# Kernel optimization log

Hardware: AMD Instinct MI355X
Metric: run time of the kernel (lower is better)

Reference implementation:

```python
import jax, jax.numpy as jnp
import numpy as np

B, N, F_IN = 32, 512, 64
HEADS = (8, 8)
HIDS = (64, 64)
EDGE_P = 0.05  # graph density
NEG_SLOPE = 0.2
NEG_INF = -1e20


def setup_inputs() -> dict:
    key = jax.random.key(0)
    ks = jax.random.split(key, 8)
    x = jax.random.normal(ks[0], (B, N, F_IN), dtype=jnp.float32)
    adj = (jax.random.uniform(ks[1], (B, N, N)) < EDGE_P).astype(jnp.float32)
    adj = jnp.maximum(adj, adj.transpose(0, 2, 1))  # symmetric adjacency
    # mask = (batch, row): every (b, n) pair gets the masked softmax
    b_idx = jnp.repeat(jnp.arange(B, dtype=jnp.int32), N)   # [B*N]
    r_idx = jnp.tile(jnp.arange(N, dtype=jnp.int32), B)     # [B*N]
    # layer 0: f_in=64 -> f_out=64, H=8 ; layer 1: f_in=64*8=512 -> f_out=64, H=8
    W0 = jax.random.normal(ks[2], (F_IN, HIDS[0]), dtype=jnp.float32) / jnp.sqrt(jnp.float32(F_IN))
    a_src0 = jax.random.normal(ks[3], (HIDS[0], HEADS[0]), dtype=jnp.float32) / jnp.sqrt(jnp.float32(HIDS[0]))
    a_dst0 = jax.random.normal(ks[4], (HIDS[0], HEADS[0]), dtype=jnp.float32) / jnp.sqrt(jnp.float32(HIDS[0]))
    f_in1 = HIDS[0] * HEADS[0]
    W1 = jax.random.normal(ks[5], (f_in1, HIDS[1]), dtype=jnp.float32) / jnp.sqrt(jnp.float32(f_in1))
    a_src1 = jax.random.normal(ks[6], (HIDS[1], HEADS[1]), dtype=jnp.float32) / jnp.sqrt(jnp.float32(HIDS[1]))
    a_dst1 = jax.random.normal(ks[7], (HIDS[1], HEADS[1]), dtype=jnp.float32) / jnp.sqrt(jnp.float32(HIDS[1]))
    return dict(x=x, adj=adj, b_idx=b_idx, r_idx=r_idx,
                W0=W0, a_src0=a_src0, a_dst0=a_dst0,
                W1=W1, a_src1=a_src1, a_dst1=a_dst1)


def _gat_layer(x, adj, b_idx, r_idx, W, a_src, a_dst):
    # x: [B,N,f_in], adj: [B,N,N] (diag already set), W: [f_in,F], a_*: [F,H]
    hp = x @ W                                        # [B,N,F]
    s = jnp.einsum('bnf,fh->bhn', hp, a_src)          # attn_src
    d = jnp.einsum('bnf,fh->bhn', hp, a_dst)          # attn_dst
    attn = s[:, :, :, None] + d[:, :, None, :]        # [B,H,N,N]
    attn = jnp.where(attn >= 0, attn, NEG_SLOPE * attn)  # leaky_relu(0.2)
    attn = jnp.where(adj[:, None, :, :] == 0, 0.0, attn)  # masked_fill(adj==0, 0)
    rows = attn[b_idx, :, r_idx, :]                   # [K,H,N]
    rows = jnp.where(rows == 0.0, NEG_INF, rows)
    rows = jax.nn.softmax(rows, axis=-1)
    attn = attn.at[b_idx, :, r_idx, :].set(rows)
    return jnp.einsum('bhij,bjf->bhif', attn, hp)     # [B,H,N,F]


def reference(x, adj, b_idx, r_idx, W0, a_src0, a_dst0, W1, a_src1, a_dst1):
    Bn, Nn = x.shape[:2]
    # torch mutates adj in place: adj[batch,row,row] = 1 (self loops)
    adj = adj.at[b_idx, r_idx, r_idx].set(1.0)
    o = _gat_layer(x, adj, b_idx, r_idx, W0, a_src0, a_dst0)      # [B,H,N,F0]
    x1 = jax.nn.elu(o.transpose(0, 2, 1, 3).reshape(Bn, Nn, -1))  # [B,N,H*F0]
    o2 = _gat_layer(x1, adj, b_idx, r_idx, W1, a_src1, a_dst1)    # [B,H,N,F1]
    return o2.mean(axis=1)                                        # [B,N,F1]
```

## Files before the change

kernel.cpp:

```cpp
#include <hip/hip_runtime.h>
#include <hip/hip_bf16.h>
#include <math.h>

#define BB 32
#define NN 512

typedef short bf16x8 __attribute__((ext_vector_type(8)));
typedef float f32x4 __attribute__((ext_vector_type(4)));

static __device__ __forceinline__ unsigned short f2bf(float v) {
    __hip_bfloat16 h = __float2bfloat16(v);
    return __builtin_bit_cast(unsigned short, h);
}
static __device__ __forceinline__ float bf2f(unsigned short u) {
    __hip_bfloat16 h = __builtin_bit_cast(__hip_bfloat16, u);
    return __bfloat162float(h);
}

__global__ __launch_bounds__(256) void k_w1t_prep(
    const float* __restrict__ W1,
    unsigned short* __restrict__ W1Th, unsigned short* __restrict__ W1Tl)
{
    int id = blockIdx.x * 256 + threadIdx.x;
    int n = id & 63, gabs = id >> 6;
    int c = gabs >> 3, gl = gabs & 7;
    int p = gl ^ (n & 7);
    bf16x8 hv, lv;
#pragma unroll
    for (int e = 0; e < 8; ++e) {
        float v = W1[(size_t)(gabs * 8 + e) * 64 + n];
        unsigned short hb = f2bf(v);
        hv[e] = (short)hb;
        lv[e] = (short)f2bf(v - bf2f(hb));
    }
    size_t g = (size_t)n * 512 + c * 64 + p * 8;
    *(bf16x8*)(W1Th + g) = hv;
    *(bf16x8*)(W1Tl + g) = lv;
}

template<int KTOT, int KCH>
__global__ __launch_bounds__(256) void k_gemm_sd(
    const float* __restrict__ X, const float* __restrict__ W,
    const float* __restrict__ a_src, const float* __restrict__ a_dst,
    float* __restrict__ s, float* __restrict__ d,
    unsigned short* __restrict__ hpT_hi, unsigned short* __restrict__ hpT_lo)
{
    constexpr int XS_STR = KCH + 4;
    __shared__ float xs[32 * XS_STR];
    __shared__ float wsh[KCH * 64];
    __shared__ float asd_f[1024];

    int t = threadIdx.x;
    int row0 = blockIdx.x * 32;
    int c = (t & 15) * 4;
    int r = (t >> 4) * 2;

    ((float4*)asd_f)[t] = (t < 128) ? ((const float4*)a_src)[t]
                                    : ((const float4*)a_dst)[t - 128];

    float acc[2][4];
#pragma unroll
    for (int u = 0; u < 4; ++u) { acc[0][u] = 0.f; acc[1][u] = 0.f; }

    for (int kc = 0; kc < KTOT / KCH; ++kc) {
        {
            int row = t >> 3;
            int kk = (t & 7) * (KCH / 8);
            const float4* xrow = (const float4*)(X + (size_t)(row0 + row) * KTOT + kc * KCH + kk);
            float4* xd = (float4*)&xs[row * XS_STR + kk];
#pragma unroll
            for (int u = 0; u < KCH / 32; ++u) xd[u] = xrow[u];
        }
#pragma unroll
        for (int u = 0; u < KCH / 16; ++u) {
            int f4 = u * 256 + t;
            int k = f4 >> 4, c4 = f4 & 15;
            ((float4*)&wsh[k * 64])[c4] =
                ((const float4*)(W + (size_t)(kc * KCH + k) * 64))[c4];
        }
        __syncthreads();
#pragma unroll 4
        for (int k = 0; k < KCH; ++k) {
            float xa = xs[r * XS_STR + k];
            float xb = xs[(r + 1) * XS_STR + k];
            float4 wv = ((const float4*)&wsh[k * 64])[c >> 2];
            acc[0][0] = fmaf(xa, wv.x, acc[0][0]);
            acc[0][1] = fmaf(xa, wv.y, acc[0][1]);
            acc[0][2] = fmaf(xa, wv.z, acc[0][2]);
            acc[0][3] = fmaf(xa, wv.w, acc[0][3]);
            acc[1][0] = fmaf(xb, wv.x, acc[1][0]);
            acc[1][1] = fmaf(xb, wv.y, acc[1][1]);
            acc[1][2] = fmaf(xb, wv.z, acc[1][2]);
            acc[1][3] = fmaf(xb, wv.w, acc[1][3]);
        }
        __syncthreads();
    }

#pragma unroll
    for (int u = 0; u < 4; ++u) {
        wsh[r * 66 + c + u]       = acc[0][u];
        wsh[(r + 1) * 66 + c + u] = acc[1][u];
    }
    __syncthreads();

    {
        int rr = t >> 3, h = t & 7;
        float sv = 0.f, dv = 0.f;
#pragma unroll
        for (int f = 0; f < 64; ++f) {
            float hv = wsh[rr * 66 + f];
            sv = fmaf(hv, asd_f[f * 8 + h], sv);
            dv = fmaf(hv, asd_f[512 + f * 8 + h], dv);
        }
        s[(size_t)(row0 + rr) * 8 + h] = sv;
        d[(size_t)(row0 + rr) * 8 + h] = dv;
    }

    {
        int b  = row0 >> 9;
        int jb = row0 & 511;
        int f = t >> 2, jl = (t & 3) * 8;
        bf16x8 hv, lv;
#pragma unroll
        for (int e = 0; e < 8; ++e) {
            float v = wsh[(jl + e) * 66 + f];
            unsigned short hb = f2bf(v);
            hv[e] = (short)hb;
            lv[e] = (short)f2bf(v - bf2f(hb));
        }
        int jj = jb + jl;
        int cch = jj >> 6, p = ((jj >> 3) & 7) ^ (f & 7);
        size_t g = ((size_t)b * 64 + f) * 512 + cch * 64 + p * 8;
        *(bf16x8*)(hpT_hi + g) = hv;
        *(bf16x8*)(hpT_lo + g) = lv;
    }
}

__global__ __launch_bounds__(256) void k_gemm1_mfma(
    const float* __restrict__ x1,
    const unsigned short* __restrict__ W1Th, const unsigned short* __restrict__ W1Tl,
    const float* __restrict__ a_src, const float* __restrict__ a_dst,
    float* __restrict__ s, float* __restrict__ d,
    unsigned short* __restrict__ hpT_hi, unsigned short* __restrict__ hpT_lo)
{
    __shared__ short Ah[32 * 64], Al[32 * 64];
    __shared__ short Bh[64 * 64], Bl[64 * 64];
    __shared__ float ctile[32 * 66];
    __shared__ float asd_f[1024];

    int t = threadIdx.x;
    int row0 = blockIdx.x * 32;
    int lane = t & 63, w = t >> 6;
    int cn = lane & 15, rq = lane >> 4;
    int rsub = (w & 1) * 16, csub = (w >> 1) * 32;

    ((float4*)asd_f)[t] = (t < 128) ? ((const float4*)a_src)[t]
                                    : ((const float4*)a_dst)[t - 128];

    f32x4 acc[2], acc2[2];
#pragma unroll
    for (int ft = 0; ft < 2; ++ft)
#pragma unroll
        for (int e = 0; e < 4; ++e) { acc[ft][e] = 0.f; acc2[ft][e] = 0.f; }

    for (int kc = 0; kc < 8; ++kc) {
        {
            int row = t >> 3, g = t & 7;
            const float4* src = (const float4*)(x1 + (size_t)(row0 + row) * 512 + kc * 64 + g * 8);
            float4 v0 = src[0], v1 = src[1];
            float vv[8] = {v0.x, v0.y, v0.z, v0.w, v1.x, v1.y, v1.z, v1.w};
            bf16x8 hv, lv;
#pragma unroll
            for (int e = 0; e < 8; ++e) {
                unsigned short hb = f2bf(vv[e]);
                hv[e] = (short)hb;
                lv[e] = (short)f2bf(vv[e] - bf2f(hb));
            }
            int p = g ^ (row & 7);
            *(bf16x8*)&Ah[row * 64 + p * 8] = hv;
            *(bf16x8*)&Al[row * 64 + p * 8] = lv;
        }
        {
            int n = t >> 2;
#pragma unroll
            for (int u = 0; u < 2; ++u) {
                int g = (t & 3) * 2 + u;
                size_t src = (size_t)n * 512 + kc * 64 + g * 8;
                *(uint4*)&Bh[n * 64 + g * 8] = *(const uint4*)(W1Th + src);
                *(uint4*)&Bl[n * 64 + g * 8] = *(const uint4*)(W1Tl + src);
            }
        }
        __syncthreads();
#pragma unroll
        for (int ks = 0; ks < 2; ++ks) {
            int m = rsub + cn;
            int pa = ((ks * 4 + rq) ^ (m & 7)) * 8;
            bf16x8 ah = *(const bf16x8*)&Ah[m * 64 + pa];
            bf16x8 al = *(const bf16x8*)&Al[m * 64 + pa];
#pragma unroll
            for (int ft = 0; ft < 2; ++ft) {
                int n = csub + ft * 16 + cn;
                int pb = ((ks * 4 + rq) ^ (n & 7)) * 8;
                bf16x8 bh = *(const bf16x8*)&Bh[n * 64 + pb];
                bf16x8 bl = *(const bf16x8*)&Bl[n * 64 + pb];
                acc[ft]  = __builtin_amdgcn_mfma_f32_16x16x32_bf16(ah, bh, acc[ft], 0, 0, 0);
                acc2[ft] = __builtin_amdgcn_mfma_f32_16x16x32_bf16(ah, bl, acc2[ft], 0, 0, 0);
                acc2[ft] = __builtin_amdgcn_mfma_f32_16x16x32_bf16(al, bh, acc2[ft], 0, 0, 0);
            }
        }
        __syncthreads();
    }

#pragma unroll
    for (int ft = 0; ft < 2; ++ft)
#pragma unroll
        for (int r = 0; r < 4; ++r) {
            int row = rsub + rq * 4 + r;
            int col = csub + ft * 16 + cn;
            ctile[row * 66 + col] = acc[ft][r] + acc2[ft][r];
        }
    __syncthreads();

    {
        int rr = t >> 3, h = t & 7;
        float sv = 0.f, dv = 0.f;
#pragma unroll
        for (int f = 0; f < 64; ++f) {
            float hv = ctile[rr * 66 + f];
            sv = fmaf(hv, asd_f[f * 8 + h], sv);
            dv = fmaf(hv, asd_f[512 + f * 8 + h], dv);
        }
        s[(size_t)(row0 + rr) * 8 + h] = sv;
        d[(size_t)(row0 + rr) * 8 + h] = dv;
    }
    {
        int b  = row0 >> 9;
        int jb = row0 & 511;
        int f = t >> 2, jl = (t & 3) * 8;
        bf16x8 hv, lv;
#pragma unroll
        for (int e = 0; e < 8; ++e) {
            float v = ctile[(jl + e) * 66 + f];
            unsigned short hb = f2bf(v);
            hv[e] = (short)hb;
            lv[e] = (short)f2bf(v - bf2f(hb));
        }
        int jj = jb + jl;
        int cch = jj >> 6, p = ((jj >> 3) & 7) ^ (f & 7);
        size_t g = ((size_t)b * 64 + f) * 512 + cch * 64 + p * 8;
        *(bf16x8*)(hpT_hi + g) = hv;
        *(bf16x8*)(hpT_lo + g) = lv;
    }
}

__global__ __launch_bounds__(256, 4) void k_attn_mfma(
    const float* __restrict__ adj, const float* __restrict__ s,
    const float* __restrict__ d,
    const unsigned short* __restrict__ hpTh,
    const unsigned short* __restrict__ hpTl,
    float* __restrict__ out, int mode)
{
    __shared__ short hT[8192];
    __shared__ float dT[8 * 68];
    __shared__ unsigned long long maskL[16];
    __shared__ float inv[128];
    float* red = (float*)hT;

    int blk = blockIdx.x;
    int vb = ((blk & 7) << 7) | (blk >> 3);
    int b = vb >> 5, i0 = (vb & 31) << 4;
    int t = threadIdx.x, lane = t & 63, w = t >> 6;
    int cn = lane & 15, rq = lane >> 4;
    int h0 = w * 2, h1 = w * 2 + 1;

    float sv0 = s[((size_t)b * NN + i0 + cn) * 8 + h0];
    float sv1 = s[((size_t)b * NN + i0 + cn) * 8 + h1];

    f32x4 acc[2][4];
#pragma unroll
    for (int hh = 0; hh < 2; ++hh)
#pragma unroll
        for (int ft = 0; ft < 4; ++ft)
#pragma unroll
            for (int e = 0; e < 4; ++e) acc[hh][ft][e] = 0.f;
    float rs0 = 0.f, rs1 = 0.f;

    for (int jc = 0; jc < NN; jc += 64) {
#pragma unroll
        for (int pp = 0; pp < 4; ++pp) {
            int row = pp * 4 + w;
            float a = adj[((size_t)b * NN + i0 + row) * NN + jc + lane];
            bool bit = (a != 0.f) || ((i0 + row) == (jc + lane));
            unsigned long long m = __ballot(bit);
            if (lane == 0) maskL[row] = m;
        }
        if (t < 128) {
            int j = t >> 1, h4 = (t & 1) * 4;
            float4 dv = *(const float4*)(d + ((size_t)b * NN + jc + j) * 8 + h4);
            dT[(h4 + 0) * 68 + j] = dv.x;
            dT[(h4 + 1) * 68 + j] = dv.y;
            dT[(h4 + 2) * 68 + j] = dv.z;
            dT[(h4 + 3) * 68 + j] = dv.w;
        }
#pragma unroll
        for (int u = 0; u < 2; ++u) {
            int idx = t + u * 256;
            int f = idx >> 3, g = idx & 7;
            size_t gaddr = ((size_t)b * 64 + f) * 512 + jc + g * 8;
            *(uint4*)&hT[f * 64 + g * 8]        = *(const uint4*)(hpTh + gaddr);
            *(uint4*)&hT[4096 + f * 64 + g * 8] = *(const uint4*)(hpTl + gaddr);
        }
        __syncthreads();

        unsigned long long mk = maskL[cn];
        bf16x8 aA[2], aB[2];
#pragma unroll
        for (int ks = 0; ks < 2; ++ks) {
            int shift = ks * 32 + rq * 8;
            unsigned int mb = (unsigned int)(mk >> shift) & 0xffu;
            const float* dp0 = &dT[h0 * 68 + shift];
            const float* dp1 = &dT[h1 * 68 + shift];
            float4 da0 = *(const float4*)dp0, da1 = *(const float4*)(dp0 + 4);
            float4 db0 = *(const float4*)dp1, db1 = *(const float4*)(dp1 + 4);
            float dd0[8] = {da0.x, da0.y, da0.z, da0.w, da1.x, da1.y, da1.z, da1.w};
            float dd1[8] = {db0.x, db0.y, db0.z, db0.w, db1.x, db1.y, db1.z, db1.w};
#pragma unroll
            for (int e = 0; e < 8; ++e) {
                bool mbit = (mb >> e) & 1;
                float e0 = sv0 + dd0[e];
                e0 = fmaxf(e0, 0.2f * e0);
                float p0 = (mbit && e0 != 0.f) ? __expf(e0) : 0.f;
                rs0 += p0;
                float e1 = sv1 + dd1[e];
                e1 = fmaxf(e1, 0.2f * e1);
                float p1 = (mbit && e1 != 0.f) ? __expf(e1) : 0.f;
                rs1 += p1;
                aA[ks][e] = (short)f2bf(p0);
                aB[ks][e] = (short)f2bf(p1);
            }
        }
#pragma unroll
        for (int ks = 0; ks < 2; ++ks)
#pragma unroll
            for (int ft = 0; ft < 4; ++ft) {
                int f = ft * 16 + cn;
                int pb = ((ks * 4 + rq) ^ (f & 7)) * 8;
                bf16x8 bh = *(const bf16x8*)&hT[f * 64 + pb];
                bf16x8 bl = *(const bf16x8*)&hT[4096 + f * 64 + pb];
                acc[0][ft] = __builtin_amdgcn_mfma_f32_16x16x32_bf16(aA[ks], bh, acc[0][ft], 0, 0, 0);
                acc[0][ft] = __builtin_amdgcn_mfma_f32_16x16x32_bf16(aA[ks], bl, acc[0][ft], 0, 0, 0);
                acc[1][ft] = __builtin_amdgcn_mfma_f32_16x16x32_bf16(aB[ks], bh, acc[1][ft], 0, 0, 0);
                acc[1][ft] = __builtin_amdgcn_mfma_f32_16x16x32_bf16(aB[ks], bl, acc[1][ft], 0, 0, 0);
            }
        __syncthreads();
    }

    rs0 += __shfl_xor(rs0, 16); rs0 += __shfl_xor(rs0, 32);
    rs1 += __shfl_xor(rs1, 16); rs1 += __shfl_xor(rs1, 32);
    if (rq == 0) {
        inv[h0 * 16 + cn] = 1.0f / rs0;
        inv[h1 * 16 + cn] = 1.0f / rs1;
    }
    __syncthreads();

    if (mode == 0) {
#pragma unroll
        for (int hh = 0; hh < 2; ++hh) {
            int h = w * 2 + hh;
#pragma unroll
            for (int ft = 0; ft < 4; ++ft)
#pragma unroll
                for (int r = 0; r < 4; ++r) {
                    int il = rq * 4 + r;
                    float v = acc[hh][ft][r] * inv[h * 16 + il];
                    v = v > 0.f ? v : __expf(v) - 1.f;
                    out[((size_t)b * NN + i0 + il) * 512 + h * 64 + ft * 16 + cn] = v;
                }
        }
    } else {
#pragma unroll
        for (int ft = 0; ft < 4; ++ft)
#pragma unroll
            for (int r = 0; r < 4; ++r) {
                int il = rq * 4 + r;
                float v = acc[0][ft][r] * inv[h0 * 16 + il]
                        + acc[1][ft][r] * inv[h1 * 16 + il];
                red[(w * 16 + il) * 64 + ft * 16 + cn] = v;
            }
        __syncthreads();
#pragma unroll
        for (int u = 0; u < 4; ++u) {
            int idx = t + u * 256;
            int il = idx >> 6, f = idx & 63;
            float sum = red[il * 64 + f] + red[(16 + il) * 64 + f]
                      + red[(32 + il) * 64 + f] + red[(48 + il) * 64 + f];
            out[((size_t)b * NN + i0 + il) * 64 + f] = sum * 0.125f;
        }
    }
}

extern "C" void kernel_launch(void* const* d_in, const int* in_sizes, int n_in,
                              void* d_out, int out_size, void* d_ws, size_t ws_size,
                              hipStream_t stream) {
    const float* x      = (const float*)d_in[0];
    const float* adj    = (const float*)d_in[1];
    const float* W0     = (const float*)d_in[4];
    const float* a_src0 = (const float*)d_in[5];
    const float* a_dst0 = (const float*)d_in[6];
    const float* W1     = (const float*)d_in[7];
    const float* a_src1 = (const float*)d_in[8];
    const float* a_dst1 = (const float*)d_in[9];
    float* out = (float*)d_out;

    float* ws = (float*)d_ws;
    const size_t R = (size_t)BB * NN;
    float* s0 = ws;
    float* d0 = s0 + R * 8;
    float* x1 = d0 + R * 8;
    float* s1 = x1 + R * 512;
    float* d1 = s1 + R * 8;
    unsigned short* hp0h = (unsigned short*)(d1 + R * 8);
    unsigned short* hp0l = hp0h + (size_t)BB * 64 * NN;
    unsigned short* hp1h = hp0l + (size_t)BB * 64 * NN;
    unsigned short* hp1l = hp1h + (size_t)BB * 64 * NN;
    unsigned short* W1Th = hp1l + (size_t)BB * 64 * NN;
    unsigned short* W1Tl = W1Th + (size_t)64 * 512;

    k_w1t_prep<<<16, 256, 0, stream>>>(W1, W1Th, W1Tl);
    k_gemm_sd<64, 64><<<512, 256, 0, stream>>>(x, W0, a_src0, a_dst0, s0, d0, hp0h, hp0l);
    k_attn_mfma<<<1024, 256, 0, stream>>>(adj, s0, d0, hp0h, hp0l, x1, 0);
    k_gemm1_mfma<<<512, 256, 0, stream>>>(x1, W1Th, W1Tl, a_src1, a_dst1, s1, d1, hp1h, hp1l);
    k_attn_mfma<<<1024, 256, 0, stream>>>(adj, s1, d1, hp1h, hp1l, out, 1);
}
```

Baseline: 183.0 us.

## Double-buffer attention tiles, MFMA layer-0 GEMM, emit split-bf16 x1 directly

The attention kernel now double-buffers the adjacency mask, d values and hp tiles in shared memory, prefetching the next 64-column chunk into registers while MFMAs run on the current one. Layer-0 GEMM moves from scalar FMA to split-bf16 MFMA with a pre-transposed W0. Layer-1 GEMM now uses 16-row tiles with register prefetch. Layer-0 attention writes x1 directly as swizzled hi/lo bf16 pairs, so the second GEMM no longer converts from fp32. Together these aim to hide global load latency and cut x1 traffic and conversion work, at the cost of doubled shared memory in the attention kernel, which may reduce occupancy.

```diff
diff --git a/kernel.cpp b/kernel.cpp
--- a/kernel.cpp
+++ b/kernel.cpp
@@ -17,211 +17,34 @@
     return __bfloat162float(h);
 }
 
-__global__ __launch_bounds__(256) void k_w1t_prep(
-    const float* __restrict__ W1,
-    unsigned short* __restrict__ W1Th, unsigned short* __restrict__ W1Tl)
+__global__ __launch_bounds__(256) void k_wt_prep(
+    const float* __restrict__ W, int KT,
+    unsigned short* __restrict__ Wh, unsigned short* __restrict__ Wl)
 {
     int id = blockIdx.x * 256 + threadIdx.x;
     int n = id & 63, gabs = id >> 6;
+    if (gabs >= (KT >> 3)) return;
     int c = gabs >> 3, gl = gabs & 7;
     int p = gl ^ (n & 7);
     bf16x8 hv, lv;
 #pragma unroll
     for (int e = 0; e < 8; ++e) {
-        float v = W1[(size_t)(gabs * 8 + e) * 64 + n];
+        float v = W[(size_t)(gabs * 8 + e) * 64 + n];
         unsigned short hb = f2bf(v);
         hv[e] = (short)hb;
         lv[e] = (short)f2bf(v - bf2f(hb));
     }
-    size_t g = (size_t)n * 512 + c * 64 + p * 8;
-    *(bf16x8*)(W1Th + g) = hv;
-    *(bf16x8*)(W1Tl + g) = lv;
-}
-
-template<int KTOT, int KCH>
-__global__ __launch_bounds__(256) void k_gemm_sd(
-    const float* __restrict__ X, const float* __restrict__ W,
-    const float* __restrict__ a_src, const float* __restrict__ a_dst,
+    size_t g = (size_t)n * KT + c * 64 + p * 8;
+    *(bf16x8*)(Wh + g) = hv;
+    *(bf16x8*)(Wl + g) = lv;
+}
+
+static __device__ __forceinline__ void epi_sd_hpt(
+    const float* ctile, const float* asd_f, int row0, int t,
     float* __restrict__ s, float* __restrict__ d,
-    unsigned short* __restrict__ hpT_hi, unsigned short* __restrict__ hpT_lo)
+    unsigned short* __restrict__ hpTh, unsigned short* __restrict__ hpTl)
 {
-    constexpr int XS_STR = KCH + 4;
-    __shared__ float xs[32 * XS_STR];
-    __shared__ float wsh[KCH * 64];
-    __shared__ float asd_f[1024];
-
-    int t = threadIdx.x;
-    int row0 = blockIdx.x * 32;
-    int c = (t & 15) * 4;
-    int r = (t >> 4) * 2;
-
-    ((float4*)asd_f)[t] = (t < 128) ? ((const float4*)a_src)[t]
-                                    : ((const float4*)a_dst)[t - 128];
-
-    float acc[2][4];
-#pragma unroll
-    for (int u = 0; u < 4; ++u) { acc[0][u] = 0.f; acc[1][u] = 0.f; }
-
-    for (int kc = 0; kc < KTOT / KCH; ++kc) {
-        {
-            int row = t >> 3;
-            int kk = (t & 7) * (KCH / 8);
-            const float4* xrow = (const float4*)(X + (size_t)(row0 + row) * KTOT + kc * KCH + kk);
-            float4* xd = (float4*)&xs[row * XS_STR + kk];
-#pragma unroll
-            for (int u = 0; u < KCH / 32; ++u) xd[u] = xrow[u];
-        }
-#pragma unroll
-        for (int u = 0; u < KCH / 16; ++u) {
-            int f4 = u * 256 + t;
-            int k = f4 >> 4, c4 = f4 & 15;
-            ((float4*)&wsh[k * 64])[c4] =
-                ((const float4*)(W + (size_t)(kc * KCH + k) * 64))[c4];
-        }
-        __syncthreads();
-#pragma unroll 4
-        for (int k = 0; k < KCH; ++k) {
-            float xa = xs[r * XS_STR + k];
-            float xb = xs[(r + 1) * XS_STR + k];
-            float4 wv = ((const float4*)&wsh[k * 64])[c >> 2];
-            acc[0][0] = fmaf(xa, wv.x, acc[0][0]);
-            acc[0][1] = fmaf(xa, wv.y, acc[0][1]);
-            acc[0][2] = fmaf(xa, wv.z, acc[0][2]);
-            acc[0][3] = fmaf(xa, wv.w, acc[0][3]);
-            acc[1][0] = fmaf(xb, wv.x, acc[1][0]);
-            acc[1][1] = fmaf(xb, wv.y, acc[1][1]);
-            acc[1][2] = fmaf(xb, wv.z, acc[1][2]);
-            acc[1][3] = fmaf(xb, wv.w, acc[1][3]);
-        }
-        __syncthreads();
-    }
-
-#pragma unroll
-    for (int u = 0; u < 4; ++u) {
-        wsh[r * 66 + c + u]       = acc[0][u];
-        wsh[(r + 1) * 66 + c + u] = acc[1][u];
-    }
-    __syncthreads();
-
-    {
-        int rr = t >> 3, h = t & 7;
-        float sv = 0.f, dv = 0.f;
-#pragma unroll
-        for (int f = 0; f < 64; ++f) {
-            float hv = wsh[rr * 66 + f];
-            sv = fmaf(hv, asd_f[f * 8 + h], sv);
-            dv = fmaf(hv, asd_f[512 + f * 8 + h], dv);
-        }
-        s[(size_t)(row0 + rr) * 8 + h] = sv;
-        d[(size_t)(row0 + rr) * 8 + h] = dv;
-    }
-
-    {
-        int b  = row0 >> 9;
-        int jb = row0 & 511;
-        int f = t >> 2, jl = (t & 3) * 8;
-        bf16x8 hv, lv;
-#pragma unroll
-        for (int e = 0; e < 8; ++e) {
-            float v = wsh[(jl + e) * 66 + f];
-            unsigned short hb = f2bf(v);
-            hv[e] = (short)hb;
-            lv[e] = (short)f2bf(v - bf2f(hb));
-        }
-        int jj = jb + jl;
-        int cch = jj >> 6, p = ((jj >> 3) & 7) ^ (f & 7);
-        size_t g = ((size_t)b * 64 + f) * 512 + cch * 64 + p * 8;
-        *(bf16x8*)(hpT_hi + g) = hv;
-        *(bf16x8*)(hpT_lo + g) = lv;
-    }
-}
-
-__global__ __launch_bounds__(256) void k_gemm1_mfma(
-    const float* __restrict__ x1,
-    const unsigned short* __restrict__ W1Th, const unsigned short* __restrict__ W1Tl,
-    const float* __restrict__ a_src, const float* __restrict__ a_dst,
-    float* __restrict__ s, float* __restrict__ d,
-    unsigned short* __restrict__ hpT_hi, unsigned short* __restrict__ hpT_lo)
-{
-    __shared__ short Ah[32 * 64], Al[32 * 64];
-    __shared__ short Bh[64 * 64], Bl[64 * 64];
-    __shared__ float ctile[32 * 66];
-    __shared__ float asd_f[1024];
-
-    int t = threadIdx.x;
-    int row0 = blockIdx.x * 32;
-    int lane = t & 63, w = t >> 6;
-    int cn = lane & 15, rq = lane >> 4;
-    int rsub = (w & 1) * 16, csub = (w >> 1) * 32;
-
-    ((float4*)asd_f)[t] = (t < 128) ? ((const float4*)a_src)[t]
-                                    : ((const float4*)a_dst)[t - 128];
-
-    f32x4 acc[2], acc2[2];
-#pragma unroll
-    for (int ft = 0; ft < 2; ++ft)
-#pragma unroll
-        for (int e = 0; e < 4; ++e) { acc[ft][e] = 0.f; acc2[ft][e] = 0.f; }
-
-    for (int kc = 0; kc < 8; ++kc) {
-        {
-            int row = t >> 3, g = t & 7;
-            const float4* src = (const float4*)(x1 + (size_t)(row0 + row) * 512 + kc * 64 + g * 8);
-            float4 v0 = src[0], v1 = src[1];
-            float vv[8] = {v0.x, v0.y, v0.z, v0.w, v1.x, v1.y, v1.z, v1.w};
-            bf16x8 hv, lv;
-#pragma unroll
-            for (int e = 0; e < 8; ++e) {
-                unsigned short hb = f2bf(vv[e]);
-                hv[e] = (short)hb;
-                lv[e] = (short)f2bf(vv[e] - bf2f(hb));
-            }
-            int p = g ^ (row & 7);
-            *(bf16x8*)&Ah[row * 64 + p * 8] = hv;
-            *(bf16x8*)&Al[row * 64 + p * 8] = lv;
-        }
-        {
-            int n = t >> 2;
-#pragma unroll
-            for (int u = 0; u < 2; ++u) {
-                int g = (t & 3) * 2 + u;
-                size_t src = (size_t)n * 512 + kc * 64 + g * 8;
-                *(uint4*)&Bh[n * 64 + g * 8] = *(const uint4*)(W1Th + src);
-                *(uint4*)&Bl[n * 64 + g * 8] = *(const uint4*)(W1Tl + src);
-            }
-        }
-        __syncthreads();
-#pragma unroll
-        for (int ks = 0; ks < 2; ++ks) {
-            int m = rsub + cn;
-            int pa = ((ks * 4 + rq) ^ (m & 7)) * 8;
-            bf16x8 ah = *(const bf16x8*)&Ah[m * 64 + pa];
-            bf16x8 al = *(const bf16x8*)&Al[m * 64 + pa];
-#pragma unroll
-            for (int ft = 0; ft < 2; ++ft) {
-                int n = csub + ft * 16 + cn;
-                int pb = ((ks * 4 + rq) ^ (n & 7)) * 8;
-                bf16x8 bh = *(const bf16x8*)&Bh[n * 64 + pb];
-                bf16x8 bl = *(const bf16x8*)&Bl[n * 64 + pb];
-                acc[ft]  = __builtin_amdgcn_mfma_f32_16x16x32_bf16(ah, bh, acc[ft], 0, 0, 0);
-                acc2[ft] = __builtin_amdgcn_mfma_f32_16x16x32_bf16(ah, bl, acc2[ft], 0, 0, 0);
-                acc2[ft] = __builtin_amdgcn_mfma_f32_16x16x32_bf16(al, bh, acc2[ft], 0, 0, 0);
-            }
-        }
-        __syncthreads();
-    }
-
-#pragma unroll
-    for (int ft = 0; ft < 2; ++ft)
-#pragma unroll
-        for (int r = 0; r < 4; ++r) {
-            int row = rsub + rq * 4 + r;
-            int col = csub + ft * 16 + cn;
-            ctile[row * 66 + col] = acc[ft][r] + acc2[ft][r];
-        }
-    __syncthreads();
-
-    {
+    if (t < 128) {
         int rr = t >> 3, h = t & 7;
         float sv = 0.f, dv = 0.f;
 #pragma unroll
@@ -232,11 +55,9 @@
         }
         s[(size_t)(row0 + rr) * 8 + h] = sv;
         d[(size_t)(row0 + rr) * 8 + h] = dv;
-    }
-    {
-        int b  = row0 >> 9;
-        int jb = row0 & 511;
-        int f = t >> 2, jl = (t & 3) * 8;
+    } else {
+        int t2 = t - 128;
+        int f = t2 >> 1, jl = (t2 & 1) * 8;
         bf16x8 hv, lv;
 #pragma unroll
         for (int e = 0; e < 8; ++e) {
@@ -245,12 +66,151 @@
             hv[e] = (short)hb;
             lv[e] = (short)f2bf(v - bf2f(hb));
         }
+        int b = row0 >> 9, jb = row0 & 511;
         int jj = jb + jl;
         int cch = jj >> 6, p = ((jj >> 3) & 7) ^ (f & 7);
         size_t g = ((size_t)b * 64 + f) * 512 + cch * 64 + p * 8;
-        *(bf16x8*)(hpT_hi + g) = hv;
-        *(bf16x8*)(hpT_lo + g) = lv;
-    }
+        *(bf16x8*)(hpTh + g) = hv;
+        *(bf16x8*)(hpTl + g) = lv;
+    }
+}
+
+__global__ __launch_bounds__(256) void k_gemm0(
+    const float* __restrict__ x,
+    const unsigned short* __restrict__ W0Th, const unsigned short* __restrict__ W0Tl,
+    const float* __restrict__ a_src, const float* __restrict__ a_dst,
+    float* __restrict__ s, float* __restrict__ d,
+    unsigned short* __restrict__ hpTh, unsigned short* __restrict__ hpTl)
+{
+    __shared__ short Ah[16 * 64], Al[16 * 64];
+    __shared__ short Bh[64 * 64], Bl[64 * 64];
+    __shared__ float ctile[16 * 66];
+    __shared__ float asd_f[1024];
+
+    int t = threadIdx.x;
+    int row0 = blockIdx.x * 16;
+
+    ((float4*)asd_f)[t] = (t < 128) ? ((const float4*)a_src)[t]
+                                    : ((const float4*)a_dst)[t - 128];
+    {
+        int n = t >> 2, gp = (t & 3) * 2;
+#pragma unroll
+        for (int u = 0; u < 2; ++u) {
+            *(uint4*)&Bh[n * 64 + (gp + u) * 8] = *(const uint4*)(W0Th + (size_t)n * 64 + (gp + u) * 8);
+            *(uint4*)&Bl[n * 64 + (gp + u) * 8] = *(const uint4*)(W0Tl + (size_t)n * 64 + (gp + u) * 8);
+        }
+    }
+    if (t < 128) {
+        int row = t >> 3, g = t & 7;
+        const float4* src = (const float4*)(x + (size_t)(row0 + row) * 64 + g * 8);
+        float4 v0 = src[0], v1 = src[1];
+        float vv[8] = {v0.x, v0.y, v0.z, v0.w, v1.x, v1.y, v1.z, v1.w};
+        bf16x8 hv, lv;
+#pragma unroll
+        for (int e = 0; e < 8; ++e) {
+            unsigned short hb = f2bf(vv[e]);
+            hv[e] = (short)hb;
+            lv[e] = (short)f2bf(vv[e] - bf2f(hb));
+        }
+        int p = g ^ (row & 7);
+        *(bf16x8*)&Ah[row * 64 + p * 8] = hv;
+        *(bf16x8*)&Al[row * 64 + p * 8] = lv;
+    }
+    __syncthreads();
+
+    int lane = t & 63, w = t >> 6, cn = lane & 15, rq = lane >> 4;
+    f32x4 acc, acc2;
+#pragma unroll
+    for (int e = 0; e < 4; ++e) { acc[e] = 0.f; acc2[e] = 0.f; }
+
+#pragma unroll
+    for (int ks = 0; ks < 2; ++ks) {
+        int pa = ((ks * 4 + rq) ^ (cn & 7)) * 8;
+        bf16x8 ah = *(const bf16x8*)&Ah[cn * 64 + pa];
+        bf16x8 al = *(const bf16x8*)&Al[cn * 64 + pa];
+        int nn = w * 16 + cn;
+        int pb = ((ks * 4 + rq) ^ (cn & 7)) * 8;
+        bf16x8 bh = *(const bf16x8*)&Bh[nn * 64 + pb];
+        bf16x8 bl = *(const bf16x8*)&Bl[nn * 64 + pb];
+        acc  = __builtin_amdgcn_mfma_f32_16x16x32_bf16(ah, bh, acc, 0, 0, 0);
+        acc2 = __builtin_amdgcn_mfma_f32_16x16x32_bf16(ah, bl, acc2, 0, 0, 0);
+        acc2 = __builtin_amdgcn_mfma_f32_16x16x32_bf16(al, bh, acc2, 0, 0, 0);
+    }
+#pragma unroll
+    for (int r = 0; r < 4; ++r)
+        ctile[(rq * 4 + r) * 66 + w * 16 + cn] = acc[r] + acc2[r];
+    __syncthreads();
+    epi_sd_hpt(ctile, asd_f, row0, t, s, d, hpTh, hpTl);
+}
+
+__global__ __launch_bounds__(256) void k_gemm1(
+    const unsigned short* __restrict__ x1h, const unsigned short* __restrict__ x1l,
+    const unsigned short* __restrict__ W1Th, const unsigned short* __restrict__ W1Tl,
+    const float* __restrict__ a_src, const float* __restrict__ a_dst,
+    float* __restrict__ s, float* __restrict__ d,
+    unsigned short* __restrict__ hpTh, unsigned short* __restrict__ hpTl)
+{
+    __shared__ short Ah[16 * 64], Al[16 * 64];
+    __shared__ short Bh[64 * 64], Bl[64 * 64];
+    __shared__ float ctile[16 * 66];
+    __shared__ float asd_f[1024];
+
+    int t = threadIdx.x;
+    int row0 = blockIdx.x * 16;
+    ((float4*)asd_f)[t] = (t < 128) ? ((const float4*)a_src)[t]
+                                    : ((const float4*)a_dst)[t - 128];
+
+    int ar = (t & 127) >> 3, ag = t & 7;
+    const unsigned short* asrc = (t < 128) ? x1h : x1l;
+    short* adst = (t < 128) ? Ah : Al;
+    int bn = t >> 2, bg0 = (t & 3) * 2;
+
+    uint4 ra, rb0, rb1, rb2, rb3;
+    ra  = *(const uint4*)(asrc + (size_t)(row0 + ar) * 512 + ag * 8);
+    rb0 = *(const uint4*)(W1Th + (size_t)bn * 512 + (bg0 + 0) * 8);
+    rb1 = *(const uint4*)(W1Th + (size_t)bn * 512 + (bg0 + 1) * 8);
+    rb2 = *(const uint4*)(W1Tl + (size_t)bn * 512 + (bg0 + 0) * 8);
+    rb3 = *(const uint4*)(W1Tl + (size_t)bn * 512 + (bg0 + 1) * 8);
+
+    int lane = t & 63, w = t >> 6, cn = lane & 15, rq = lane >> 4;
+    f32x4 acc, acc2;
+#pragma unroll
+    for (int e = 0; e < 4; ++e) { acc[e] = 0.f; acc2[e] = 0.f; }
+
+    for (int kc = 0; kc < 8; ++kc) {
+        *(uint4*)&adst[ar * 64 + ag * 8] = ra;
+        *(uint4*)&Bh[bn * 64 + (bg0 + 0) * 8] = rb0;
+        *(uint4*)&Bh[bn * 64 + (bg0 + 1) * 8] = rb1;
+        *(uint4*)&Bl[bn * 64 + (bg0 + 0) * 8] = rb2;
+        *(uint4*)&Bl[bn * 64 + (bg0 + 1) * 8] = rb3;
+        __syncthreads();
+        if (kc < 7) {
+            int k0 = (kc + 1) * 64;
+            ra  = *(const uint4*)(asrc + (size_t)(row0 + ar) * 512 + k0 + ag * 8);
+            rb0 = *(const uint4*)(W1Th + (size_t)bn * 512 + k0 + (bg0 + 0) * 8);
+            rb1 = *(const uint4*)(W1Th + (size_t)bn * 512 + k0 + (bg0 + 1) * 8);
+            rb2 = *(const uint4*)(W1Tl + (size_t)bn * 512 + k0 + (bg0 + 0) * 8);
+            rb3 = *(const uint4*)(W1Tl + (size_t)bn * 512 + k0 + (bg0 + 1) * 8);
+        }
+#pragma unroll
+        for (int ks = 0; ks < 2; ++ks) {
+            int pa = ((ks * 4 + rq) ^ (cn & 7)) * 8;
+            bf16x8 ah = *(const bf16x8*)&Ah[cn * 64 + pa];
+            bf16x8 al = *(const bf16x8*)&Al[cn * 64 + pa];
+            int nn = w * 16 + cn;
+            bf16x8 bh = *(const bf16x8*)&Bh[nn * 64 + pa];
+            bf16x8 bl = *(const bf16x8*)&Bl[nn * 64 + pa];
+            acc  = __builtin_amdgcn_mfma_f32_16x16x32_bf16(ah, bh, acc, 0, 0, 0);
+            acc2 = __builtin_amdgcn_mfma_f32_16x16x32_bf16(ah, bl, acc2, 0, 0, 0);
+            acc2 = __builtin_amdgcn_mfma_f32_16x16x32_bf16(al, bh, acc2, 0, 0, 0);
+        }
+        __syncthreads();
+    }
+#pragma unroll
+    for (int r = 0; r < 4; ++r)
+        ctile[(rq * 4 + r) * 66 + w * 16 + cn] = acc[r] + acc2[r];
+    __syncthreads();
+    epi_sd_hpt(ctile, asd_f, row0, t, s, d, hpTh, hpTl);
 }
 
 __global__ __launch_bounds__(256, 4) void k_attn_mfma(
@@ -258,24 +218,54 @@
     const float* __restrict__ d,
     const unsigned short* __restrict__ hpTh,
     const unsigned short* __restrict__ hpTl,
-    float* __restrict__ out, int mode)
+    unsigned short* __restrict__ o_h, unsigned short* __restrict__ o_l,
+    float* __restrict__ o_f, int mode)
 {
-    __shared__ short hT[8192];
-    __shared__ float dT[8 * 68];
-    __shared__ unsigned long long maskL[16];
+    __shared__ short hT[2][8192];
+    __shared__ float dT[2][8 * 68];
+    __shared__ unsigned long long maskL[2][16];
     __shared__ float inv[128];
-    float* red = (float*)hT;
+    float* red = (float*)&hT[0][0];
 
     int blk = blockIdx.x;
     int vb = ((blk & 7) << 7) | (blk >> 3);
     int b = vb >> 5, i0 = (vb & 31) << 4;
     int t = threadIdx.x, lane = t & 63, w = t >> 6;
     int cn = lane & 15, rq = lane >> 4;
-    int h0 = w * 2, h1 = w * 2 + 1;
+    int h0 = w * 2, h1 = h0 + 1;
 
     float sv0 = s[((size_t)b * NN + i0 + cn) * 8 + h0];
     float sv1 = s[((size_t)b * NN + i0 + cn) * 8 + h1];
 
+    const float* adjb = adj + ((size_t)b * NN + i0) * NN;
+    const unsigned short* hbh = hpTh + (size_t)b * 64 * 512;
+    const unsigned short* hbl = hpTl + (size_t)b * 64 * 512;
+
+#pragma unroll
+    for (int pp = 0; pp < 4; ++pp) {
+        int row = pp * 4 + w;
+        float a = adjb[(size_t)row * NN + lane];
+        bool bit = (a != 0.f) || ((i0 + row) == lane);
+        unsigned long long m = __ballot(bit);
+        if (lane == 0) maskL[0][row] = m;
+    }
+    if (t < 128) {
+        int j = t >> 1, h4 = (t & 1) * 4;
+        float4 dv = *(const float4*)(d + ((size_t)b * NN + j) * 8 + h4);
+        dT[0][(h4 + 0) * 68 + j] = dv.x;
+        dT[0][(h4 + 1) * 68 + j] = dv.y;
+        dT[0][(h4 + 2) * 68 + j] = dv.z;
+        dT[0][(h4 + 3) * 68 + j] = dv.w;
+    }
+#pragma unroll
+    for (int u = 0; u < 2; ++u) {
+        int idx = t + u * 256;
+        int f = idx >> 3, g = idx & 7;
+        *(uint4*)&hT[0][f * 64 + g * 8]        = *(const uint4*)(hbh + (size_t)f * 512 + g * 8);
+        *(uint4*)&hT[0][4096 + f * 64 + g * 8] = *(const uint4*)(hbl + (size_t)f * 512 + g * 8);
+    }
+    __syncthreads();
+
     f32x4 acc[2][4];
 #pragma unroll
     for (int hh = 0; hh < 2; ++hh)
@@ -285,41 +275,39 @@
             for (int e = 0; e < 4; ++e) acc[hh][ft][e] = 0.f;
     float rs0 = 0.f, rs1 = 0.f;
 
-    for (int jc = 0; jc < NN; jc += 64) {
-#pragma unroll
-        for (int pp = 0; pp < 4; ++pp) {
-            int row = pp * 4 + w;
-            float a = adj[((size_t)b * NN + i0 + row) * NN + jc + lane];
-            bool bit = (a != 0.f) || ((i0 + row) == (jc + lane));
-            unsigned long long m = __ballot(bit);
-            if (lane == 0) maskL[row] = m;
-        }
-        if (t < 128) {
-            int j = t >> 1, h4 = (t & 1) * 4;
-            float4 dv = *(const float4*)(d + ((size_t)b * NN + jc + j) * 8 + h4);
-            dT[(h4 + 0) * 68 + j] = dv.x;
-            dT[(h4 + 1) * 68 + j] = dv.y;
-            dT[(h4 + 2) * 68 + j] = dv.z;
-            dT[(h4 + 3) * 68 + j] = dv.w;
-        }
-#pragma unroll
-        for (int u = 0; u < 2; ++u) {
-            int idx = t + u * 256;
-            int f = idx >> 3, g = idx & 7;
-            size_t gaddr = ((size_t)b * 64 + f) * 512 + jc + g * 8;
-            *(uint4*)&hT[f * 64 + g * 8]        = *(const uint4*)(hpTh + gaddr);
-            *(uint4*)&hT[4096 + f * 64 + g * 8] = *(const uint4*)(hpTl + gaddr);
-        }
-        __syncthreads();
-
-        unsigned long long mk = maskL[cn];
+    for (int jcx = 0; jcx < 8; ++jcx) {
+        int cur = jcx & 1, nxt = cur ^ 1;
+        int jcn = (jcx + 1) * 64;
+        bool pf = jcx < 7;
+        float pa[4];
+        float4 pd;
+        uint4 ph0, ph1, pl0, pl1;
+        if (pf) {
+#pragma unroll
+            for (int pp = 0; pp < 4; ++pp)
+                pa[pp] = adjb[(size_t)(pp * 4 + w) * NN + jcn + lane];
+            if (t < 128) {
+                int j = t >> 1, h4 = (t & 1) * 4;
+                pd = *(const float4*)(d + ((size_t)b * NN + jcn + j) * 8 + h4);
+            }
+            {
+                int f0 = t >> 3, g0 = t & 7;
+                int f1 = (t + 256) >> 3, g1 = t & 7;
+                ph0 = *(const uint4*)(hbh + (size_t)f0 * 512 + jcn + g0 * 8);
+                pl0 = *(const uint4*)(hbl + (size_t)f0 * 512 + jcn + g0 * 8);
+                ph1 = *(const uint4*)(hbh + (size_t)f1 * 512 + jcn + g1 * 8);
+                pl1 = *(const uint4*)(hbl + (size_t)f1 * 512 + jcn + g1 * 8);
+            }
+        }
+
+        unsigned long long mk = maskL[cur][cn];
         bf16x8 aA[2], aB[2];
 #pragma unroll
         for (int ks = 0; ks < 2; ++ks) {
             int shift = ks * 32 + rq * 8;
             unsigned int mb = (unsigned int)(mk >> shift) & 0xffu;
-            const float* dp0 = &dT[h0 * 68 + shift];
-            const float* dp1 = &dT[h1 * 68 + shift];
+            const float* dp0 = &dT[cur][h0 * 68 + shift];
+            const float* dp1 = &dT[cur][h1 * 68 + shift];
             float4 da0 = *(const float4*)dp0, da1 = *(const float4*)(dp0 + 4);
             float4 db0 = *(const float4*)dp1, db1 = *(const float4*)(dp1 + 4);
             float dd0[8] = {da0.x, da0.y, da0.z, da0.w, da1.x, da1.y, da1.z, da1.w};
@@ -345,13 +333,38 @@
             for (int ft = 0; ft < 4; ++ft) {
                 int f = ft * 16 + cn;
                 int pb = ((ks * 4 + rq) ^ (f & 7)) * 8;
-                bf16x8 bh = *(const bf16x8*)&hT[f * 64 + pb];
-                bf16x8 bl = *(const bf16x8*)&hT[4096 + f * 64 + pb];
+                bf16x8 bh = *(const bf16x8*)&hT[cur][f * 64 + pb];
+                bf16x8 bl = *(const bf16x8*)&hT[cur][4096 + f * 64 + pb];
                 acc[0][ft] = __builtin_amdgcn_mfma_f32_16x16x32_bf16(aA[ks], bh, acc[0][ft], 0, 0, 0);
                 acc[0][ft] = __builtin_amdgcn_mfma_f32_16x16x32_bf16(aA[ks], bl, acc[0][ft], 0, 0, 0);
                 acc[1][ft] = __builtin_amdgcn_mfma_f32_16x16x32_bf16(aB[ks], bh, acc[1][ft], 0, 0, 0);
                 acc[1][ft] = __builtin_amdgcn_mfma_f32_16x16x32_bf16(aB[ks], bl, acc[1][ft], 0, 0, 0);
             }
+
+        if (pf) {
+#pragma unroll
+            for (int pp = 0; pp < 4; ++pp) {
+                int row = pp * 4 + w;
+                bool bit = (pa[pp] != 0.f) || ((i0 + row) == (jcn + lane));
+                unsigned long long m = __ballot(bit);
+                if (lane == 0) maskL[nxt][row] = m;
+            }
+            if (t < 128) {
+                int j = t >> 1, h4 = (t & 1) * 4;
+                dT[nxt][(h4 + 0) * 68 + j] = pd.x;
+                dT[nxt][(h4 + 1) * 68 + j] = pd.y;
+                dT[nxt][(h4 + 2) * 68 + j] = pd.z;
+                dT[nxt][(h4 + 3) * 68 + j] = pd.w;
+            }
+            {
+                int f0 = t >> 3, g0 = t & 7;
+                int f1 = (t + 256) >> 3;
+                *(uint4*)&hT[nxt][f0 * 64 + g0 * 8]        = ph0;
+                *(uint4*)&hT[nxt][4096 + f0 * 64 + g0 * 8] = pl0;
+                *(uint4*)&hT[nxt][f1 * 64 + g0 * 8]        = ph1;
+                *(uint4*)&hT[nxt][4096 + f1 * 64 + g0 * 8] = pl1;
+            }
+        }
         __syncthreads();
     }
 
@@ -366,7 +379,7 @@
     if (mode == 0) {
 #pragma unroll
         for (int hh = 0; hh < 2; ++hh) {
-            int h = w * 2 + hh;
+            int h = h0 + hh;
 #pragma unroll
             for (int ft = 0; ft < 4; ++ft)
 #pragma unroll
@@ -374,7 +387,12 @@
                     int il = rq * 4 + r;
                     float v = acc[hh][ft][r] * inv[h * 16 + il];
                     v = v > 0.f ? v : __expf(v) - 1.f;
-                    out[((size_t)b * NN + i0 + il) * 512 + h * 64 + ft * 16 + cn] = v;
+                    int g = ft * 2 + (cn >> 3);
+                    int p = g ^ (il & 7);
+                    size_t addr = ((size_t)b * NN + i0 + il) * 512 + h * 64 + p * 8 + (cn & 7);
+                    unsigned short hb = f2bf(v);
+                    o_h[addr] = hb;
+                    o_l[addr] = f2bf(v - bf2f(hb));
                 }
         }
     } else {
@@ -394,7 +412,7 @@
             int il = idx >> 6, f = idx & 63;
             float sum = red[il * 64 + f] + red[(16 + il) * 64 + f]
                       + red[(32 + il) * 64 + f] + red[(48 + il) * 64 + f];
-            out[((size_t)b * NN + i0 + il) * 64 + f] = sum * 0.125f;
+            o_f[((size_t)b * NN + i0 + il) * 64 + f] = sum * 0.125f;
         }
     }
 }
@@ -416,19 +434,23 @@
     const size_t R = (size_t)BB * NN;
     float* s0 = ws;
     float* d0 = s0 + R * 8;
-    float* x1 = d0 + R * 8;
-    float* s1 = x1 + R * 512;
+    float* s1 = d0 + R * 8;
     float* d1 = s1 + R * 8;
-    unsigned short* hp0h = (unsigned short*)(d1 + R * 8);
+    unsigned short* x1h  = (unsigned short*)(d1 + R * 8);
+    unsigned short* x1l  = x1h + R * 512;
+    unsigned short* hp0h = x1l + R * 512;
     unsigned short* hp0l = hp0h + (size_t)BB * 64 * NN;
     unsigned short* hp1h = hp0l + (size_t)BB * 64 * NN;
     unsigned short* hp1l = hp1h + (size_t)BB * 64 * NN;
-    unsigned short* W1Th = hp1l + (size_t)BB * 64 * NN;
+    unsigned short* W0Th = hp1l + (size_t)BB * 64 * NN;
+    unsigned short* W0Tl = W0Th + (size_t)64 * 64;
+    unsigned short* W1Th = W0Tl + (size_t)64 * 64;
     unsigned short* W1Tl = W1Th + (size_t)64 * 512;
 
-    k_w1t_prep<<<16, 256, 0, stream>>>(W1, W1Th, W1Tl);
-    k_gemm_sd<64, 64><<<512, 256, 0, stream>>>(x, W0, a_src0, a_dst0, s0, d0, hp0h, hp0l);
-    k_attn_mfma<<<1024, 256, 0, stream>>>(adj, s0, d0, hp0h, hp0l, x1, 0);
-    k_gemm1_mfma<<<512, 256, 0, stream>>>(x1, W1Th, W1Tl, a_src1, a_dst1, s1, d1, hp1h, hp1l);
-    k_attn_mfma<<<1024, 256, 0, stream>>>(adj, s1, d1, hp1h, hp1l, out, 1);
-}
+    k_wt_prep<<<2, 256, 0, stream>>>(W0, 64, W0Th, W0Tl);
+    k_wt_prep<<<16, 256, 0, stream>>>(W1, 512, W1Th, W1Tl);
+    k_gemm0<<<1024, 256, 0, stream>>>(x, W0Th, W0Tl, a_src0, a_dst0, s0, d0, hp0h, hp0l);
+    k_attn_mfma<<<1024, 256, 0, stream>>>(adj, s0, d0, hp0h, hp0l, x1h, x1l, nullptr, 0);
+    k_gemm1<<<1024, 256, 0, stream>>>(x1h, x1l, W1Th, W1Tl, a_src1, a_dst1, s1, d1, hp1h, hp1l);
+    k_attn_mfma<<<1024, 256, 0, stream>>>(adj, s1, d1, hp1h, hp1l, nullptr, nullptr, out, 1);
+}
```

Result: slower. 190.8 us (+4.3%).
